# Performance work log

Hardware: AMD Instinct MI355X
Metric: run time of the kernel (lower is better)

Reference implementation:

```python
import jax, jax.numpy as jnp
import numpy as np

M_ROWS = 65536
LENGTH = 512


def setup_inputs() -> dict:
    key = jax.random.key(0)
    k1, k2 = jax.random.split(key)
    x = jax.random.normal(k1, (M_ROWS, LENGTH), dtype=jnp.float32)
    mask = jax.random.uniform(k2, (M_ROWS, LENGTH), dtype=jnp.float32)
    return {"x": x, "mask": mask}


def reference(x, mask):
    # regular_matrix M has M[j,j]=1 (j>=1, M[0,0]=0) and M[j-1,j]=-1,
    # so (x @ M)[:, 0] = 0 and (x @ M)[:, j] = x[:, j] - x[:, j-1] for j >= 1.
    diff = x[:, 1:] - x[:, :-1]                      # [m, n-1]
    product = jnp.pad(diff, ((0, 0), (1, 0)))        # column 0 is zero
    loss = (jax.nn.relu(jnp.abs(product) - 1.0) * mask).sum()
    return loss
```

## Files before the change

kernel.cpp:

```cpp
#include <hip/hip_runtime.h>

#define M_ROWS 65536
#define LENGTH 512
#define NBLOCKS 2048
#define BLOCK 256

__global__ __launch_bounds__(BLOCK) void connect_loss_partial(
    const float* __restrict__ x,
    const float* __restrict__ mask,
    float* __restrict__ part) {
  const int wave = threadIdx.x >> 6;
  const int lane = threadIdx.x & 63;
  const int waves_total = gridDim.x * (BLOCK / 64);
  float acc = 0.0f;

  for (int row = blockIdx.x * (BLOCK / 64) + wave; row < M_ROWS; row += waves_total) {
    const float4* xr = reinterpret_cast<const float4*>(x + (size_t)row * LENGTH) + lane * 2;
    const float4* mr = reinterpret_cast<const float4*>(mask + (size_t)row * LENGTH) + lane * 2;
    float4 a0 = xr[0];
    float4 a1 = xr[1];
    float4 m0 = mr[0];
    float4 m1 = mr[1];

    float prev = __shfl_up(a1.w, 1);

    float v[8] = {a0.x, a0.y, a0.z, a0.w, a1.x, a1.y, a1.z, a1.w};
    float m[8] = {m0.x, m0.y, m0.z, m0.w, m1.x, m1.y, m1.z, m1.w};

    float p = (lane == 0) ? v[0] : prev;
#pragma unroll
    for (int c = 0; c < 8; ++c) {
      float d = v[c] - p;
      p = v[c];
      float t = fabsf(d) - 1.0f;
      acc += (t > 0.0f ? t : 0.0f) * m[c];
    }
  }

#pragma unroll
  for (int off = 32; off; off >>= 1) acc += __shfl_down(acc, off);

  __shared__ float s[BLOCK / 64];
  if (lane == 0) s[wave] = acc;
  __syncthreads();
  if (threadIdx.x == 0) part[blockIdx.x] = s[0] + s[1] + s[2] + s[3];
}

__global__ __launch_bounds__(BLOCK) void connect_loss_reduce(
    const float* __restrict__ part, float* __restrict__ out, int n) {
  const int wave = threadIdx.x >> 6;
  const int lane = threadIdx.x & 63;
  float acc = 0.0f;
  for (int i = threadIdx.x; i < n; i += BLOCK) acc += part[i];
#pragma unroll
  for (int off = 32; off; off >>= 1) acc += __shfl_down(acc, off);
  __shared__ float s[BLOCK / 64];
  if (lane == 0) s[wave] = acc;
  __syncthreads();
  if (threadIdx.x == 0) out[0] = s[0] + s[1] + s[2] + s[3];
}

extern "C" void kernel_launch(void* const* d_in, const int* in_sizes, int n_in,
                              void* d_out, int out_size, void* d_ws, size_t ws_size,
                              hipStream_t stream) {
  const float* x = (const float*)d_in[0];
  const float* mask = (const float*)d_in[1];
  float* out = (float*)d_out;
  float* part = (float*)d_ws;

  connect_loss_partial<<<NBLOCKS, BLOCK, 0, stream>>>(x, mask, part);
  connect_loss_reduce<<<1, BLOCK, 0, stream>>>(part, out, NBLOCKS);
}
```

Measured before the change: 46.76 us.

## Assign two rows per wave with coalesced float4 loads and no grid-stride loop

Each wave now handles two full rows (1024 floats). Every lane issues four contiguous float4 loads per tensor, so each wave-wide load is a contiguous 1 KB segment, and all eight loads are issued up front to increase memory-level parallelism. The grid-stride loop is removed and the grid grows to 8192 blocks, which exactly covers 65536 rows. Row boundaries are handled with shuffles. The final reduce kernel now reads partials as float4. The design hardcodes the shape, so it is only correct when rows are an exact multiple of the wave coverage.

```diff
diff --git a/kernel.cpp b/kernel.cpp
--- a/kernel.cpp
+++ b/kernel.cpp
@@ -2,39 +2,60 @@
 
 #define M_ROWS 65536
 #define LENGTH 512
-#define NBLOCKS 2048
 #define BLOCK 256
+#define NBLOCKS 8192
+
+__device__ __forceinline__ void chunk_acc(float& acc, float4 v, float4 m, float p0) {
+  float t;
+  t = fabsf(v.x - p0) - 1.0f;  acc += fmaxf(t, 0.0f) * m.x;
+  t = fabsf(v.y - v.x) - 1.0f; acc += fmaxf(t, 0.0f) * m.y;
+  t = fabsf(v.z - v.y) - 1.0f; acc += fmaxf(t, 0.0f) * m.z;
+  t = fabsf(v.w - v.z) - 1.0f; acc += fmaxf(t, 0.0f) * m.w;
+}
 
 __global__ __launch_bounds__(BLOCK) void connect_loss_partial(
     const float* __restrict__ x,
     const float* __restrict__ mask,
     float* __restrict__ part) {
+  const int lane = threadIdx.x & 63;
   const int wave = threadIdx.x >> 6;
-  const int lane = threadIdx.x & 63;
-  const int waves_total = gridDim.x * (BLOCK / 64);
+  const size_t wave_base = ((size_t)blockIdx.x * (BLOCK / 64) + wave) * 1024;
+
+  const float4* xb = reinterpret_cast<const float4*>(x + wave_base);
+  const float4* mb = reinterpret_cast<const float4*>(mask + wave_base);
+
+  float4 v0 = xb[lane];
+  float4 v1 = xb[64 + lane];
+  float4 v2 = xb[128 + lane];
+  float4 v3 = xb[192 + lane];
+  float4 m0 = mb[lane];
+  float4 m1 = mb[64 + lane];
+  float4 m2 = mb[128 + lane];
+  float4 m3 = mb[192 + lane];
+
   float acc = 0.0f;
 
-  for (int row = blockIdx.x * (BLOCK / 64) + wave; row < M_ROWS; row += waves_total) {
-    const float4* xr = reinterpret_cast<const float4*>(x + (size_t)row * LENGTH) + lane * 2;
-    const float4* mr = reinterpret_cast<const float4*>(mask + (size_t)row * LENGTH) + lane * 2;
-    float4 a0 = xr[0];
-    float4 a1 = xr[1];
-    float4 m0 = mr[0];
-    float4 m1 = mr[1];
-
-    float prev = __shfl_up(a1.w, 1);
-
-    float v[8] = {a0.x, a0.y, a0.z, a0.w, a1.x, a1.y, a1.z, a1.w};
-    float m[8] = {m0.x, m0.y, m0.z, m0.w, m1.x, m1.y, m1.z, m1.w};
-
-    float p = (lane == 0) ? v[0] : prev;
-#pragma unroll
-    for (int c = 0; c < 8; ++c) {
-      float d = v[c] - p;
-      p = v[c];
-      float t = fabsf(d) - 1.0f;
-      acc += (t > 0.0f ? t : 0.0f) * m[c];
-    }
+  {
+    float p = __shfl_up(v0.w, 1);
+    if (lane == 0) p = v0.x;
+    chunk_acc(acc, v0, m0, p);
+  }
+  {
+    float p = __shfl_up(v1.w, 1);
+    float last = __shfl(v0.w, 63);
+    if (lane == 0) p = last;
+    chunk_acc(acc, v1, m1, p);
+  }
+  {
+    float p = __shfl_up(v2.w, 1);
+    if (lane == 0) p = v2.x;
+    chunk_acc(acc, v2, m2, p);
+  }
+  {
+    float p = __shfl_up(v3.w, 1);
+    float last = __shfl(v2.w, 63);
+    if (lane == 0) p = last;
+    chunk_acc(acc, v3, m3, p);
   }
 
 #pragma unroll
@@ -51,7 +72,11 @@
   const int wave = threadIdx.x >> 6;
   const int lane = threadIdx.x & 63;
   float acc = 0.0f;
-  for (int i = threadIdx.x; i < n; i += BLOCK) acc += part[i];
+  const float4* p4 = reinterpret_cast<const float4*>(part);
+  for (int i = threadIdx.x; i < n / 4; i += BLOCK) {
+    float4 v = p4[i];
+    acc += (v.x + v.y) + (v.z + v.w);
+  }
 #pragma unroll
   for (int off = 32; off; off >>= 1) acc += __shfl_down(acc, off);
   __shared__ float s[BLOCK / 64];
```

After: 46.98 us. Within noise of the previous version (+0.5%).
